# Optimization experiments

Hardware: AMD Instinct MI355X
Metric: run time of the kernel (lower is better)

Reference implementation:

```python
import jax, jax.numpy as jnp
import numpy as np

TAF = 0.05
EPS = 1e-8  # matches torch CosineSimilarity default eps

def _normalize(x):
    # torch cosine sim divides by max(||x||, eps) per vector
    n = jnp.linalg.norm(x, axis=-1, keepdims=True)
    return x / jnp.maximum(n, EPS)

def setup_inputs() -> dict:
    key = jax.random.key(0)
    k1, k2, k3 = jax.random.split(key, 3)
    N, D = 8192, 128
    return {
        "z": jax.random.normal(k1, (N, D), dtype=jnp.float32),
        "z_p": jax.random.normal(k2, (N, D), dtype=jnp.float32),
        "z_n": jax.random.normal(k3, (N, D), dtype=jnp.float32),
    }

def reference(z, z_p, z_n):
    # Fused normalize + matmul instead of broadcasting [N, M, D] intermediates.
    zn = _normalize(z)
    p_sim = zn @ _normalize(z_p).T / TAF   # [N, M]
    n_sim = zn @ _normalize(z_n).T / TAF   # [N, K]
    logits = jnp.concatenate([p_sim, n_sim], axis=1)  # [N, M+K]
    labels = jnp.arange(logits.shape[0])
    logp = jax.nn.log_softmax(logits, axis=-1)
    loss = -jnp.mean(jnp.take_along_axis(logp, labels[:, None], axis=1))
    return loss
```

## Files before the change

### kernel.cpp

```cpp
#include <hip/hip_runtime.h>
#include <hip/hip_bf16.h>
#include <stdint.h>


#define TAF_F 0.05f
constexpr float LOG2E  = 1.4426950408889634f;
constexpr float SCALE  = LOG2E / TAF_F;
constexpr float OFFSET = -20.0f * LOG2E;

constexpr int N_ROWS     = 8192;
constexpr int D_DIM      = 128;
constexpr int TWO_N      = 16384;
constexpr int NJ         = 32;
constexpr int JCHUNK     = TWO_N / NJ;
constexpr int BN_TILE    = 64;
constexpr int NT         = JCHUNK / BN_TILE;
constexpr int BLOCK_ROWS = 256;
constexpr int WAVE_ROWS  = 64;
constexpr int TILE_BYTES = BN_TILE * D_DIM * 2;

typedef __bf16 bf16x8 __attribute__((ext_vector_type(8)));
typedef __bf16 bf16x2 __attribute__((ext_vector_type(2)));
typedef float  f32x4  __attribute__((ext_vector_type(4)));

typedef __attribute__((address_space(3))) uint32_t       lds_u32;
typedef const __attribute__((address_space(1))) uint32_t glb_u32;

#if __has_builtin(__builtin_amdgcn_exp2f)
#define EXP2(x) __builtin_amdgcn_exp2f(x)
#else
#define EXP2(x) exp2f(x)
#endif

__global__ void normalize_diag_kernel(const float* __restrict__ z,
                                      const float* __restrict__ zp,
                                      const float* __restrict__ znm,
                                      __bf16* __restrict__ znb,
                                      __bf16* __restrict__ bnb,
                                      float* __restrict__ diag) {
    const int wv   = threadIdx.x >> 6;
    const int lane = threadIdx.x & 63;
    const int i    = blockIdx.x * 4 + wv;

    const float2 vz = *reinterpret_cast<const float2*>(z   + (size_t)i * D_DIM + lane * 2);
    const float2 vp = *reinterpret_cast<const float2*>(zp  + (size_t)i * D_DIM + lane * 2);
    const float2 vn = *reinterpret_cast<const float2*>(znm + (size_t)i * D_DIM + lane * 2);

    float sz  = vz.x * vz.x + vz.y * vz.y;
    float sp  = vp.x * vp.x + vp.y * vp.y;
    float sn  = vn.x * vn.x + vn.y * vn.y;
    float szp = vz.x * vp.x + vz.y * vp.y;
#pragma unroll
    for (int o = 32; o >= 1; o >>= 1) {
        sz  += __shfl_xor(sz, o);
        sp  += __shfl_xor(sp, o);
        sn  += __shfl_xor(sn, o);
        szp += __shfl_xor(szp, o);
    }
    const float rz = 1.0f / fmaxf(sqrtf(sz), 1e-8f);
    const float rp = 1.0f / fmaxf(sqrtf(sp), 1e-8f);
    const float rn = 1.0f / fmaxf(sqrtf(sn), 1e-8f);

    bf16x2 oz = { (__bf16)(vz.x * rz), (__bf16)(vz.y * rz) };
    bf16x2 op = { (__bf16)(vp.x * rp), (__bf16)(vp.y * rp) };
    bf16x2 on = { (__bf16)(vn.x * rn), (__bf16)(vn.y * rn) };
    *reinterpret_cast<bf16x2*>(znb + (size_t)i * D_DIM + lane * 2)            = oz;
    *reinterpret_cast<bf16x2*>(bnb + (size_t)i * D_DIM + lane * 2)            = op;
    *reinterpret_cast<bf16x2*>(bnb + (size_t)(N_ROWS + i) * D_DIM + lane * 2) = on;
    if (lane == 0) diag[i] = szp * rz * rp * (1.0f / TAF_F);
}

__global__ __launch_bounds__(256, 2) void partial_lse_kernel(
        const __bf16* __restrict__ znb,
        const __bf16* __restrict__ bnb,
        float* __restrict__ partial) {
    __shared__ __align__(16) unsigned char lds[TILE_BYTES * 2];

    const int tid  = threadIdx.x;
    const int lane = tid & 63;
    const int wv   = tid >> 6;
    const int l15  = lane & 15;
    const int l4   = lane >> 4;
    const int rowBase = blockIdx.x * BLOCK_ROWS + wv * WAVE_ROWS;
    const int jBase   = blockIdx.y * JCHUNK;

    const unsigned char* srcBase = reinterpret_cast<const unsigned char*>(bnb);

    auto stage = [&](int tile, int buf) {
        const unsigned char* srcTile = srcBase + (size_t)(jBase + tile * BN_TILE) * 256;
        unsigned char* ldsw = lds + buf * TILE_BYTES;
#pragma unroll
        for (int it = 0; it < 4; ++it) {
            const int s = it * 256 + tid;
            const int g = s ^ ((s >> 4) & 7);
            __builtin_amdgcn_global_load_lds(
                (glb_u32*)(srcTile + (size_t)g * 16),
                (lds_u32*)(ldsw + s * 16), 16, 0, 0);
        }
    };

    bf16x8 a[4][4];
#pragma unroll
    for (int s = 0; s < 4; ++s)
#pragma unroll
        for (int kk = 0; kk < 4; ++kk) {
            const __bf16* p = znb + (size_t)(rowBase + s * 16 + l15) * D_DIM + kk * 32 + l4 * 8;
            a[s][kk] = *reinterpret_cast<const bf16x8*>(p);
        }

    float sums[4][4];
#pragma unroll
    for (int s = 0; s < 4; ++s)
#pragma unroll
        for (int e = 0; e < 4; ++e) sums[s][e] = 0.0f;

    stage(0, 0);

    for (int jt = 0; jt < NT; ++jt) {
        __syncthreads();

        if (jt + 1 < NT) stage(jt + 1, (jt + 1) & 1);

        const unsigned char* ldsr = lds + (jt & 1) * TILE_BYTES;
#pragma unroll
        for (int jsub = 0; jsub < 4; ++jsub) {
            bf16x8 b[4];
            const int r = jsub * 16 + l15;
#pragma unroll
            for (int kk = 0; kk < 4; ++kk) {
                const int cl = r * 16 + kk * 4 + l4;
                const int ca = cl ^ (r & 7);
                b[kk] = *reinterpret_cast<const bf16x8*>(ldsr + ca * 16);
            }
#pragma unroll
            for (int s = 0; s < 4; ++s) {
                f32x4 acc = {0.0f, 0.0f, 0.0f, 0.0f};
#pragma unroll
                for (int kk = 0; kk < 4; ++kk)
                    acc = __builtin_amdgcn_mfma_f32_16x16x32_bf16(a[s][kk], b[kk], acc, 0, 0, 0);
#pragma unroll
                for (int e = 0; e < 4; ++e)
                    sums[s][e] += EXP2(fmaf(acc[e], SCALE, OFFSET));
            }
        }
    }

#pragma unroll
    for (int s = 0; s < 4; ++s)
#pragma unroll
        for (int e = 0; e < 4; ++e) {
            float v = sums[s][e];
            v += __shfl_xor(v, 1);
            v += __shfl_xor(v, 2);
            v += __shfl_xor(v, 4);
            v += __shfl_xor(v, 8);
            sums[s][e] = v;
        }
    if (l15 == 0) {
#pragma unroll
        for (int s = 0; s < 4; ++s)
#pragma unroll
            for (int e = 0; e < 4; ++e) {
                const int row = rowBase + s * 16 + l4 * 4 + e;
                partial[(size_t)row * NJ + blockIdx.y] = sums[s][e];
            }
    }
}

__global__ void finalize_rows_kernel(const float* __restrict__ partial,
                                     const float* __restrict__ diag,
                                     float* __restrict__ blocksum) {
    const int t = threadIdx.x;
    const int r = blockIdx.x * 256 + t;
    const float4* prow = reinterpret_cast<const float4*>(partial + (size_t)r * NJ);
    float se = 0.0f;
#pragma unroll
    for (int c = 0; c < NJ / 4; ++c) {
        const float4 v = prow[c];
        se += (v.x + v.y) + (v.z + v.w);
    }
    float res = 20.0f + logf(se) - diag[r];
#pragma unroll
    for (int o = 32; o >= 1; o >>= 1) res += __shfl_xor(res, o);
    __shared__ float red[4];
    if ((t & 63) == 0) red[t >> 6] = res;
    __syncthreads();
    if (t == 0) blocksum[blockIdx.x] = red[0] + red[1] + red[2] + red[3];
}

__global__ void final_kernel(const float* __restrict__ blocksum,
                             float* __restrict__ out) {
    const int t = threadIdx.x;
    float v = (t < 32) ? blocksum[t] : 0.0f;
#pragma unroll
    for (int o = 32; o >= 1; o >>= 1) v += __shfl_xor(v, o);
    if (t == 0) out[0] = v * (1.0f / (float)N_ROWS);
}

extern "C" void kernel_launch(void* const* d_in, const int* in_sizes, int n_in,
                              void* d_out, int out_size, void* d_ws, size_t ws_size,
                              hipStream_t stream) {
    const float* z   = (const float*)d_in[0];
    const float* zp  = (const float*)d_in[1];
    const float* znm = (const float*)d_in[2];

    char* ws = (char*)d_ws;
    __bf16* znb     = (__bf16*)(ws);
    __bf16* bnb     = (__bf16*)(ws + 2097152);
    float*  diag    = (float*)(ws + 6291456);
    float*  partial = (float*)(ws + 6324224);
    float*  blocksum= (float*)(ws + 7372800);
    float*  out     = (float*)d_out;

    normalize_diag_kernel<<<N_ROWS / 4, 256, 0, stream>>>(z, zp, znm, znb, bnb, diag);
    partial_lse_kernel<<<dim3(N_ROWS / BLOCK_ROWS, NJ), 256, 0, stream>>>(znb, bnb, partial);
    finalize_rows_kernel<<<N_ROWS / 256, 256, 0, stream>>>(partial, diag, blocksum);
    final_kernel<<<1, 64, 0, stream>>>(blocksum, out);
}
```

Baseline: 52.97 us.

## Load B fragments directly from global into registers, dropping LDS staging

The partial LSE kernel no longer stages B tiles into shared memory with global_load_lds and block barriers. Each wave now loads its B fragments straight from global memory (L2/cache) into registers, double-buffered in software, and the block-level syncthreads calls are gone. Occupancy hint raised from 2 to 3 blocks per CU. This trades barrier and LDS traffic for redundant global loads, since all four waves read the same B data, and the loads are less coalesced with 16-byte strided accesses.

```diff
diff --git a/kernel.cpp b/kernel.cpp
--- a/kernel.cpp
+++ b/kernel.cpp
@@ -13,18 +13,13 @@
 constexpr int TWO_N      = 16384;
 constexpr int NJ         = 32;
 constexpr int JCHUNK     = TWO_N / NJ;
-constexpr int BN_TILE    = 64;
-constexpr int NT         = JCHUNK / BN_TILE;
+constexpr int NSUB       = JCHUNK / 16;
 constexpr int BLOCK_ROWS = 256;
 constexpr int WAVE_ROWS  = 64;
-constexpr int TILE_BYTES = BN_TILE * D_DIM * 2;
 
 typedef __bf16 bf16x8 __attribute__((ext_vector_type(8)));
 typedef __bf16 bf16x2 __attribute__((ext_vector_type(2)));
 typedef float  f32x4  __attribute__((ext_vector_type(4)));
-
-typedef __attribute__((address_space(3))) uint32_t       lds_u32;
-typedef const __attribute__((address_space(1))) uint32_t glb_u32;
 
 #if __has_builtin(__builtin_amdgcn_exp2f)
 #define EXP2(x) __builtin_amdgcn_exp2f(x)
@@ -70,12 +65,10 @@
     if (lane == 0) diag[i] = szp * rz * rp * (1.0f / TAF_F);
 }
 
-__global__ __launch_bounds__(256, 2) void partial_lse_kernel(
+__global__ __launch_bounds__(256, 3) void partial_lse_kernel(
         const __bf16* __restrict__ znb,
         const __bf16* __restrict__ bnb,
         float* __restrict__ partial) {
-    __shared__ __align__(16) unsigned char lds[TILE_BYTES * 2];
-
     const int tid  = threadIdx.x;
     const int lane = tid & 63;
     const int wv   = tid >> 6;
@@ -83,21 +76,6 @@
     const int l4   = lane >> 4;
     const int rowBase = blockIdx.x * BLOCK_ROWS + wv * WAVE_ROWS;
     const int jBase   = blockIdx.y * JCHUNK;
-
-    const unsigned char* srcBase = reinterpret_cast<const unsigned char*>(bnb);
-
-    auto stage = [&](int tile, int buf) {
-        const unsigned char* srcTile = srcBase + (size_t)(jBase + tile * BN_TILE) * 256;
-        unsigned char* ldsw = lds + buf * TILE_BYTES;
-#pragma unroll
-        for (int it = 0; it < 4; ++it) {
-            const int s = it * 256 + tid;
-            const int g = s ^ ((s >> 4) & 7);
-            __builtin_amdgcn_global_load_lds(
-                (glb_u32*)(srcTile + (size_t)g * 16),
-                (lds_u32*)(ldsw + s * 16), 16, 0, 0);
-        }
-    };
 
     bf16x8 a[4][4];
 #pragma unroll
@@ -114,35 +92,34 @@
 #pragma unroll
         for (int e = 0; e < 4; ++e) sums[s][e] = 0.0f;
 
-    stage(0, 0);
+    const unsigned char* bp = reinterpret_cast<const unsigned char*>(bnb)
+                            + (size_t)(jBase + l15) * 256 + l4 * 16;
 
-    for (int jt = 0; jt < NT; ++jt) {
-        __syncthreads();
+    auto loadB = [&](int js, bf16x8* b) {
+#pragma unroll
+        for (int kk = 0; kk < 4; ++kk)
+            b[kk] = *reinterpret_cast<const bf16x8*>(bp + (size_t)js * 4096 + kk * 64);
+    };
+    auto compute = [&](const bf16x8* b) {
+#pragma unroll
+        for (int s = 0; s < 4; ++s) {
+            f32x4 acc = {0.0f, 0.0f, 0.0f, 0.0f};
+#pragma unroll
+            for (int kk = 0; kk < 4; ++kk)
+                acc = __builtin_amdgcn_mfma_f32_16x16x32_bf16(a[s][kk], b[kk], acc, 0, 0, 0);
+#pragma unroll
+            for (int e = 0; e < 4; ++e)
+                sums[s][e] += EXP2(fmaf(acc[e], SCALE, OFFSET));
+        }
+    };
 
-        if (jt + 1 < NT) stage(jt + 1, (jt + 1) & 1);
-
-        const unsigned char* ldsr = lds + (jt & 1) * TILE_BYTES;
-#pragma unroll
-        for (int jsub = 0; jsub < 4; ++jsub) {
-            bf16x8 b[4];
-            const int r = jsub * 16 + l15;
-#pragma unroll
-            for (int kk = 0; kk < 4; ++kk) {
-                const int cl = r * 16 + kk * 4 + l4;
-                const int ca = cl ^ (r & 7);
-                b[kk] = *reinterpret_cast<const bf16x8*>(ldsr + ca * 16);
-            }
-#pragma unroll
-            for (int s = 0; s < 4; ++s) {
-                f32x4 acc = {0.0f, 0.0f, 0.0f, 0.0f};
-#pragma unroll
-                for (int kk = 0; kk < 4; ++kk)
-                    acc = __builtin_amdgcn_mfma_f32_16x16x32_bf16(a[s][kk], b[kk], acc, 0, 0, 0);
-#pragma unroll
-                for (int e = 0; e < 4; ++e)
-                    sums[s][e] += EXP2(fmaf(acc[e], SCALE, OFFSET));
-            }
-        }
+    bf16x8 b0[4], b1[4];
+    loadB(0, b0);
+    for (int js = 0; js < NSUB; js += 2) {
+        loadB(js + 1, b1);
+        compute(b0);
+        loadB((js + 2) & (NSUB - 1), b0);
+        compute(b1);
     }
 
 #pragma unroll
```

Measured after the change: 86.44 us. +63.2%, slower.

## Interleave per-chunk async loads with MFMA, swizzle block order, raise compute priority

Applied to the files above, without the earlier changes.

The main loop now splits each tile load into four chunks and issues the load for the next tile's chunk inside each 16-column sub-step. It waits on a partial vmcnt plus a barrier per sub-step instead of one full sync per tile. Block IDs are flattened and swizzled so blocks sharing a column chunk (XCD-aware mapping by bid&7) run together, which should improve L2 reuse. s_setprio is raised around the MFMA/exp section. This adds more barriers per tile. Issuing a wraparound dummy load on the last tile means some redundant traffic.

```diff
diff --git a/kernel.cpp b/kernel.cpp
--- a/kernel.cpp
+++ b/kernel.cpp
@@ -81,22 +81,23 @@
     const int wv   = tid >> 6;
     const int l15  = lane & 15;
     const int l4   = lane >> 4;
-    const int rowBase = blockIdx.x * BLOCK_ROWS + wv * WAVE_ROWS;
-    const int jBase   = blockIdx.y * JCHUNK;
+
+    const int bid = blockIdx.x;
+    const int swz = (bid & 7) * 128 + (bid >> 3);
+    const int rowBlk = swz & 31;
+    const int jChunk = swz >> 5;
+    const int rowBase = rowBlk * BLOCK_ROWS + wv * WAVE_ROWS;
+    const int jBase   = jChunk * JCHUNK;
 
     const unsigned char* srcBase = reinterpret_cast<const unsigned char*>(bnb);
 
-    auto stage = [&](int tile, int buf) {
+    auto stageChunk = [&](int tile, int buf, int j) {
         const unsigned char* srcTile = srcBase + (size_t)(jBase + tile * BN_TILE) * 256;
-        unsigned char* ldsw = lds + buf * TILE_BYTES;
-#pragma unroll
-        for (int it = 0; it < 4; ++it) {
-            const int s = it * 256 + tid;
-            const int g = s ^ ((s >> 4) & 7);
-            __builtin_amdgcn_global_load_lds(
-                (glb_u32*)(srcTile + (size_t)g * 16),
-                (lds_u32*)(ldsw + s * 16), 16, 0, 0);
-        }
+        const int s = j * 256 + tid;
+        const int g = s ^ ((s >> 4) & 7);
+        __builtin_amdgcn_global_load_lds(
+            (glb_u32*)(srcTile + (size_t)g * 16),
+            (lds_u32*)(lds + buf * TILE_BYTES + s * 16), 16, 0, 0);
     };
 
     bf16x8 a[4][4];
@@ -114,24 +115,32 @@
 #pragma unroll
         for (int e = 0; e < 4; ++e) sums[s][e] = 0.0f;
 
-    stage(0, 0);
+#pragma unroll
+    for (int j = 0; j < 4; ++j) stageChunk(0, 0, j);
 
     for (int jt = 0; jt < NT; ++jt) {
-        __syncthreads();
-
-        if (jt + 1 < NT) stage(jt + 1, (jt + 1) & 1);
-
-        const unsigned char* ldsr = lds + (jt & 1) * TILE_BYTES;
-#pragma unroll
-        for (int jsub = 0; jsub < 4; ++jsub) {
+        const int cur = jt & 1;
+        const unsigned char* ldsr = lds + cur * TILE_BYTES;
+        const int nxtTile = (jt + 1) & (NT - 1);
+        const int nxtBuf  = cur ^ 1;
+#pragma unroll
+        for (int j = 0; j < 4; ++j) {
+            asm volatile("s_waitcnt vmcnt(3)" ::: "memory");
+            __builtin_amdgcn_s_barrier();
+            __builtin_amdgcn_sched_barrier(0);
+
             bf16x8 b[4];
-            const int r = jsub * 16 + l15;
+            const int r = j * 16 + l15;
 #pragma unroll
             for (int kk = 0; kk < 4; ++kk) {
                 const int cl = r * 16 + kk * 4 + l4;
                 const int ca = cl ^ (r & 7);
                 b[kk] = *reinterpret_cast<const bf16x8*>(ldsr + ca * 16);
             }
+
+            stageChunk(nxtTile, nxtBuf, j);
+
+            __builtin_amdgcn_s_setprio(1);
 #pragma unroll
             for (int s = 0; s < 4; ++s) {
                 f32x4 acc = {0.0f, 0.0f, 0.0f, 0.0f};
@@ -142,8 +151,10 @@
                 for (int e = 0; e < 4; ++e)
                     sums[s][e] += EXP2(fmaf(acc[e], SCALE, OFFSET));
             }
+            __builtin_amdgcn_s_setprio(0);
         }
     }
+    asm volatile("s_waitcnt vmcnt(0)" ::: "memory");
 
 #pragma unroll
     for (int s = 0; s < 4; ++s)
@@ -162,7 +173,7 @@
 #pragma unroll
             for (int e = 0; e < 4; ++e) {
                 const int row = rowBase + s * 16 + l4 * 4 + e;
-                partial[(size_t)row * NJ + blockIdx.y] = sums[s][e];
+                partial[(size_t)row * NJ + jChunk] = sums[s][e];
             }
     }
 }
@@ -213,7 +224,7 @@
     float*  out     = (float*)d_out;
 
     normalize_diag_kernel<<<N_ROWS / 4, 256, 0, stream>>>(z, zp, znm, znb, bnb, diag);
-    partial_lse_kernel<<<dim3(N_ROWS / BLOCK_ROWS, NJ), 256, 0, stream>>>(znb, bnb, partial);
+    partial_lse_kernel<<<NJ * (N_ROWS / BLOCK_ROWS), 256, 0, stream>>>(znb, bnb, partial);
     finalize_rows_kernel<<<N_ROWS / 256, 256, 0, stream>>>(partial, diag, blocksum);
     final_kernel<<<1, 64, 0, stream>>>(blocksum, out);
 }
```

Result: slower. 54.72 us (+3.3%).
